# Kernel optimization log

Hardware: AMD Instinct MI355X
Metric: run time of the kernel (lower is better)

## Reference

```python
import jax, jax.numpy as jnp
import numpy as np

DIM, HEADS, HD = 1536, 12, 128
B, F, H, W = 1, 8, 16, 28
L = F * H * W  # 3584
EPS = 1e-6


def setup_inputs() -> dict:
    key = jax.random.key(0)
    ks = jax.random.split(key, 8)
    s = 0.02
    x = jax.random.normal(ks[0], (B, L, DIM), jnp.float32)
    # RoPE tables: angles pos * theta_j, shape [1024, HD//2]
    ang = jnp.arange(1024, dtype=jnp.float32)[:, None] / (
        10000.0 ** (jnp.arange(HD // 2, dtype=jnp.float32) / (HD // 2)))
    freqs_cos = jnp.cos(ang)
    freqs_sin = jnp.sin(ang)
    Wq = jax.random.normal(ks[1], (DIM, DIM), jnp.float32) * s
    Wk = jax.random.normal(ks[2], (DIM, DIM), jnp.float32) * s
    Wv = jax.random.normal(ks[3], (DIM, DIM), jnp.float32) * s
    Wo = jax.random.normal(ks[4], (DIM, DIM), jnp.float32) * s
    zb = jnp.zeros((DIM,), jnp.float32)
    return dict(x=x, freqs_cos=freqs_cos, freqs_sin=freqs_sin,
                Wq=Wq, bq=zb, Wk=Wk, bk=zb, Wv=Wv, bv=zb, Wo=Wo, bo=zb,
                gq=jnp.ones((DIM,), jnp.float32), gk=jnp.ones((DIM,), jnp.float32),
                f=F, h=H, w=W)


def rms_norm(t, g, eps=EPS):
    # WanRMSNorm: x * rsqrt(mean(x^2) + eps) * weight, over last dim (full `dim`)
    return t * jax.lax.rsqrt(jnp.mean(t * t, axis=-1, keepdims=True) + eps) * g


def rope_apply(t, f, h, w, cos, sin):
    # t: [B, L, H, D]; 3D rope with per-axis frequency splits [c-2(c//3), c//3, c//3]
    B_, L_, H_, D_ = t.shape
    c = D_ // 2
    s0 = c - 2 * (c // 3)
    s1 = c // 3

    def build(tab):
        tf = jnp.broadcast_to(tab[:f, :s0][:, None, None, :], (f, h, w, s0))
        th = jnp.broadcast_to(tab[:h, s0:s0 + s1][None, :, None, :], (f, h, w, s1))
        tw = jnp.broadcast_to(tab[:w, s0 + s1:c][None, None, :, :], (f, h, w, s1))
        return jnp.concatenate([tf, th, tw], axis=-1).reshape(f * h * w, c)[:L_]

    cs = build(cos)[None, :, None, :]  # [1, L, 1, c]
    sn = build(sin)[None, :, None, :]
    tp = t.reshape(B_, L_, H_, c, 2)   # consecutive pairs -> complex (re, im)
    tr, ti = tp[..., 0], tp[..., 1]
    out_r = tr * cs - ti * sn
    out_i = tr * sn + ti * cs
    return jnp.stack([out_r, out_i], axis=-1).reshape(B_, L_, H_, D_)


def reference(x, freqs_cos, freqs_sin, Wq, bq, Wk, bk, Wv, bv, Wo, bo, gq, gk, f, h, w):
    B_, L_, _ = x.shape
    q = rms_norm(x @ Wq.T + bq, gq).reshape(B_, L_, HEADS, HD)
    k = rms_norm(x @ Wk.T + bk, gk).reshape(B_, L_, HEADS, HD)
    v = (x @ Wv.T + bv).reshape(B_, L_, HEADS, HD)
    q = rope_apply(q, f, h, w, freqs_cos, freqs_sin)
    k = rope_apply(k, f, h, w, freqs_cos, freqs_sin)
    scale = 1.0 / np.sqrt(HD).astype(np.float32)
    att = jax.nn.softmax(jnp.einsum('bqhd,bkhd->bhqk', q, k) * scale, axis=-1)
    o = jnp.einsum('bhqk,bkhd->bqhd', att, v).reshape(B_, L_, DIM)
    return o @ Wo.T + bo
```

## Files before the change

### kernel.cpp

```cpp
#include <hip/hip_runtime.h>
#include <hip/hip_bf16.h>


#define DIM   1536
#define HEADS 12
#define HD    128
#define LSEQ  3584

typedef __bf16 bf16_t;
typedef __attribute__((ext_vector_type(8))) __bf16 bf16x8;
typedef __attribute__((ext_vector_type(4))) float f32x4;
typedef __attribute__((ext_vector_type(16))) float f32x16;
typedef unsigned int u32;
typedef __attribute__((ext_vector_type(2))) unsigned int u32x2;
typedef __attribute__((ext_vector_type(4))) unsigned int u32x4;

static __device__ __forceinline__ ushort f2bf(float f) {
  bf16_t h = (bf16_t)f;
  return __builtin_bit_cast(ushort, h);
}
static __device__ __forceinline__ float bf2f(ushort u) {
  return (float)__builtin_bit_cast(bf16_t, u);
}
static __device__ __forceinline__ u32 pkbf(float a, float b) {
  return (u32)f2bf(a) | ((u32)f2bf(b) << 16);
}

static __device__ __forceinline__ void plswap(u32& x, u32& y, int hi) {
#if __has_builtin(__builtin_amdgcn_permlane32_swap)
  (void)hi;
  u32x2 r = __builtin_amdgcn_permlane32_swap(x, y, false, false);
  x = r[0]; y = r[1];
#else
  u32 sx = __shfl_xor(x, 32, 64);
  u32 sy = __shfl_xor(y, 32, 64);
  u32 nx = hi ? sy : x;
  u32 ny = hi ? y : sx;
  x = nx; y = ny;
#endif
}

__global__ __launch_bounds__(256) void cvt_f32_bf16(const float* __restrict__ in,
                                                    ushort* __restrict__ out, int n) {
  int i = (blockIdx.x * 256 + threadIdx.x) * 4;
  if (i + 3 < n) {
    float4 v = *reinterpret_cast<const float4*>(in + i);
    ushort4 o;
    o.x = f2bf(v.x); o.y = f2bf(v.y); o.z = f2bf(v.z); o.w = f2bf(v.w);
    *reinterpret_cast<ushort4*>(out + i) = o;
  }
}

template <int SEGS, bool OUT_F32>
__global__ __launch_bounds__(256) void gemm_bt(const ushort* __restrict__ A,
                                               const ushort* __restrict__ B,
                                               const float* __restrict__ bias0,
                                               const float* __restrict__ bias1,
                                               const float* __restrict__ bias2,
                                               void* __restrict__ Cout) {
  const int K = DIM;
  __shared__ __attribute__((aligned(16))) ushort As[128 * 32];
  __shared__ __attribute__((aligned(16))) ushort Bs[128 * 32];
  const int tid  = threadIdx.x;
  const int lane = tid & 63;
  const int wid  = tid >> 6;
  const int m0 = blockIdx.x * 128;
  const int n0 = blockIdx.y * 128;
  const int wm = (wid >> 1) * 64;
  const int wn = (wid & 1) * 64;
  const int lr = lane & 15;
  const int lg = lane >> 4;
  const int crow = lane >> 2;
  const int ccol = (lane & 3) * 8;

  f32x4 acc[4][4] = {};

  for (int kt = 0; kt < K; kt += 32) {
    __syncthreads();
#pragma unroll
    for (int i = 0; i < 2; ++i) {
      int chunk = wid * 2 + i;
      int row = chunk * 16 + crow;
      const ushort* ga = A + (size_t)(m0 + row) * K + kt + ccol;
      const ushort* gb = B + (size_t)(n0 + row) * K + kt + ccol;
      __builtin_amdgcn_global_load_lds(
          (__attribute__((address_space(1))) void*)(void*)ga,
          (__attribute__((address_space(3))) void*)(&As[chunk * 512]), 16, 0, 0);
      __builtin_amdgcn_global_load_lds(
          (__attribute__((address_space(1))) void*)(void*)gb,
          (__attribute__((address_space(3))) void*)(&Bs[chunk * 512]), 16, 0, 0);
    }
    __syncthreads();

    bf16x8 af[4], bfr[4];
#pragma unroll
    for (int m = 0; m < 4; ++m)
      af[m] = *reinterpret_cast<const bf16x8*>(&As[(wm + m * 16 + lr) * 32 + lg * 8]);
#pragma unroll
    for (int n = 0; n < 4; ++n)
      bfr[n] = *reinterpret_cast<const bf16x8*>(&Bs[(wn + n * 16 + lr) * 32 + lg * 8]);
#pragma unroll
    for (int m = 0; m < 4; ++m)
#pragma unroll
      for (int n = 0; n < 4; ++n)
        acc[m][n] = __builtin_amdgcn_mfma_f32_16x16x32_bf16(af[m], bfr[n], acc[m][n], 0, 0, 0);
  }

  int seg = 0;
  const float* bp = bias0;
  if (SEGS == 3) {
    seg = n0 >= 2 * DIM ? 2 : (n0 >= DIM ? 1 : 0);
    bp = seg == 0 ? bias0 : (seg == 1 ? bias1 : bias2);
  }
  const int nbase = n0 - seg * DIM;

#pragma unroll
  for (int m = 0; m < 4; ++m) {
#pragma unroll
    for (int n = 0; n < 4; ++n) {
      int col = nbase + wn + n * 16 + lr;
      float bvv = bp[col];
#pragma unroll
      for (int r = 0; r < 4; ++r) {
        int row = m0 + wm + m * 16 + lg * 4 + r;
        float v = acc[m][n][r] + bvv;
        if (OUT_F32)
          ((float*)Cout)[(size_t)row * DIM + col] = v;
        else
          ((ushort*)Cout)[(size_t)seg * ((size_t)LSEQ * DIM) + (size_t)row * DIM + col] = f2bf(v);
      }
    }
  }
}

__global__ __launch_bounds__(256) void normrope(ushort* __restrict__ Qb,
                                                ushort* __restrict__ Kb,
                                                const float* __restrict__ gq,
                                                const float* __restrict__ gk,
                                                const float* __restrict__ cosT,
                                                const float* __restrict__ sinT) {
  __shared__ float red[4];
  const int l = blockIdx.x;
  const int tid = threadIdx.x;
  ushort* row = (blockIdx.y == 0 ? Qb : Kb) + (size_t)l * DIM;
  const float* g = blockIdx.y == 0 ? gq : gk;

  const u32* rp = reinterpret_cast<const u32*>(row);
  u32 pk[3];
  float v[6];
#pragma unroll
  for (int i = 0; i < 3; ++i) {
    pk[i] = rp[tid * 3 + i];
    v[2 * i]     = bf2f((ushort)(pk[i] & 0xffff));
    v[2 * i + 1] = bf2f((ushort)(pk[i] >> 16));
  }
  float ss = 0.f;
#pragma unroll
  for (int i = 0; i < 6; ++i) ss += v[i] * v[i];
#pragma unroll
  for (int off = 1; off < 64; off <<= 1) ss += __shfl_xor(ss, off, 64);
  if ((tid & 63) == 0) red[tid >> 6] = ss;
  __syncthreads();
  float tot = red[0] + red[1] + red[2] + red[3];
  float rms = rsqrtf(tot * (1.0f / DIM) + 1e-6f);

  const int fi = l / 448;
  const int rem = l % 448;
  const int hi = rem / 28;
  const int wi = rem % 28;

  u32* wp = reinterpret_cast<u32*>(row);
#pragma unroll
  for (int i = 0; i < 3; ++i) {
    int p = tid * 3 + i;
    int head = p >> 6;
    int j = p & 63;
    int trow = (j < 22) ? fi : ((j < 43) ? hi : wi);
    float cv = cosT[trow * 64 + j];
    float sv = sinT[trow * 64 + j];
    int idx = head * 128 + 2 * j;
    float xr = v[2 * i] * rms * g[idx];
    float xi = v[2 * i + 1] * rms * g[idx + 1];
    float orr = xr * cv - xi * sv;
    float oii = xr * sv + xi * cv;
    wp[p] = (u32)f2bf(orr) | ((u32)f2bf(oii) << 16);
  }
}

#define QBLK 128
#define KVB  64

__global__ __launch_bounds__(256, 2) void attn(const ushort* __restrict__ Q,
                                               const ushort* __restrict__ Kp,
                                               const ushort* __restrict__ Vp,
                                               ushort* __restrict__ O,
                                               float* __restrict__ Opart,
                                               float* __restrict__ mlbuf) {
  __shared__ __attribute__((aligned(16))) ushort Ks[2][KVB * 128];
  __shared__ __attribute__((aligned(16))) ushort Vt[2][128][72];
  const int tid  = threadIdx.x;
  const int lane = tid & 63;
  const int wv   = tid >> 6;
  const int lq   = lane & 31;
  const int hi   = lane >> 5;
  const int h    = blockIdx.y;
  const int q0   = blockIdx.x * QBLK;
  const float scale = 0.08838834764831845f;

  const int split  = blockIdx.z;
  const int nsplit = gridDim.z;
  const int NT     = LSEQ / KVB;
  const int t_lo   = split * NT / nsplit;
  const int t_hi   = (split + 1) * NT / nsplit;

  bf16x8 qf[8];
  {
    const ushort* qbase = Q + (size_t)(q0 + wv * 32 + lq) * DIM + h * HD;
#pragma unroll
    for (int d = 0; d < 8; ++d)
      qf[d] = *reinterpret_cast<const bf16x8*>(qbase + d * 16 + hi * 8);
  }

  f32x16 accO[4] = {};
  float m = -1e30f, lsum = 0.f;

  const int mbk = tid >> 4;
  const int mbd = tid & 15;

  uint4 vr0, vr1, vr2, vr3;
  auto issueK = [&](int t, int nb) {
    const int kv0 = t * KVB;
#pragma unroll
    for (int i = 0; i < 4; ++i) {
      int o16 = (wv * 4 + i) * 64 + lane;
      int r = o16 >> 4;
      int b = (o16 & 15) * 16;
      int srcu = (b ^ ((r & 7) << 4)) >> 1;
      const ushort* gp = Kp + (size_t)(kv0 + r) * DIM + h * HD + srcu;
      __builtin_amdgcn_global_load_lds(
          (__attribute__((address_space(1))) void*)(void*)gp,
          (__attribute__((address_space(3))) void*)(&Ks[nb][(wv * 4 + i) * 512]), 16, 0, 0);
    }
  };
  auto loadV = [&](int t) {
    const ushort* vbase = Vp + (size_t)(t * KVB + mbk * 4) * DIM + h * HD + mbd * 8;
    vr0 = *reinterpret_cast<const uint4*>(vbase);
    vr1 = *reinterpret_cast<const uint4*>(vbase + DIM);
    vr2 = *reinterpret_cast<const uint4*>(vbase + 2 * DIM);
    vr3 = *reinterpret_cast<const uint4*>(vbase + 3 * DIM);
  };
  auto writeV = [&](int nb) {
    const ushort* s0 = reinterpret_cast<const ushort*>(&vr0);
    const ushort* s1 = reinterpret_cast<const ushort*>(&vr1);
    const ushort* s2 = reinterpret_cast<const ushort*>(&vr2);
    const ushort* s3 = reinterpret_cast<const ushort*>(&vr3);
#pragma unroll
    for (int jj = 0; jj < 8; ++jj) {
      int j = (jj + mbd) & 7;
      uint2 w;
      w.x = (u32)s0[j] | ((u32)s1[j] << 16);
      w.y = (u32)s2[j] | ((u32)s3[j] << 16);
      *reinterpret_cast<uint2*>(&Vt[nb][mbd * 8 + j][mbk * 4]) = w;
    }
  };

  issueK(t_lo, 0);
  loadV(t_lo);

  int buf = 0;
  for (int t = t_lo; t < t_hi; ++t) {
    writeV(buf);
    __syncthreads();

    if (t + 1 < t_hi) {
      issueK(t + 1, buf ^ 1);
      loadV(t + 1);
    }

#pragma unroll
    for (int hf = 0; hf < 2; ++hf) {
      f32x16 sv = {};
      __builtin_amdgcn_s_setprio(1);
#pragma unroll
      for (int d = 0; d < 8; ++d) {
        int db = d * 32 + hi * 16;
        const bf16x8 a = *reinterpret_cast<const bf16x8*>(
            (const char*)&Ks[buf][0] + (hf * 32 + lq) * 256 + (db ^ ((lq & 7) << 4)));
        sv = __builtin_amdgcn_mfma_f32_32x32x16_bf16(a, qf[d], sv, 0, 0, 0);
      }
      __builtin_amdgcn_s_setprio(0);

      float pmax = sv[0];
#pragma unroll
      for (int r = 1; r < 16; ++r) pmax = fmaxf(pmax, sv[r]);
      pmax = fmaxf(pmax, __shfl_xor(pmax, 32, 64));
      pmax *= scale;

      if (__any(pmax > m + 8.f)) {
        float mn = fmaxf(m, pmax);
        float al = __expf(m - mn);
        m = mn;
        lsum *= al;
#pragma unroll
        for (int r = 0; r < 16; ++r) {
          int qr = (r & 3) + 8 * (r >> 2) + 4 * hi;
          float alr = __shfl(al, qr, 64);
          accO[0][r] *= alr; accO[1][r] *= alr;
          accO[2][r] *= alr; accO[3][r] *= alr;
        }
      }

      float p[16];
      float psum = 0.f;
#pragma unroll
      for (int r = 0; r < 16; ++r) {
        p[r] = __expf(fmaf(sv[r], scale, -m));
        psum += p[r];
      }
      psum += __shfl_xor(psum, 32, 64);
      lsum += psum;

      u32 a0 = pkbf(p[0], p[1]),   a1 = pkbf(p[2], p[3]);
      u32 a4 = pkbf(p[4], p[5]),   a5 = pkbf(p[6], p[7]);
      u32 c0 = pkbf(p[8], p[9]),   c1 = pkbf(p[10], p[11]);
      u32 c4 = pkbf(p[12], p[13]), c5 = pkbf(p[14], p[15]);
      plswap(a0, a4, hi);
      plswap(a1, a5, hi);
      plswap(c0, c4, hi);
      plswap(c1, c5, hi);
      u32x4 w0 = {a0, a1, a4, a5};
      u32x4 w1 = {c0, c1, c4, c5};
      bf16x8 pa0 = __builtin_bit_cast(bf16x8, w0);
      bf16x8 pa1 = __builtin_bit_cast(bf16x8, w1);

      __builtin_amdgcn_s_setprio(1);
#pragma unroll
      for (int nd = 0; nd < 4; ++nd) {
        bf16x8 vb0 = *reinterpret_cast<const bf16x8*>(
            &Vt[buf][nd * 32 + lq][hf * 32 + hi * 8]);
        accO[nd] = __builtin_amdgcn_mfma_f32_32x32x16_bf16(pa0, vb0, accO[nd], 0, 0, 0);
      }
#pragma unroll
      for (int nd = 0; nd < 4; ++nd) {
        bf16x8 vb1 = *reinterpret_cast<const bf16x8*>(
            &Vt[buf][nd * 32 + lq][hf * 32 + 16 + hi * 8]);
        accO[nd] = __builtin_amdgcn_mfma_f32_32x32x16_bf16(pa1, vb1, accO[nd], 0, 0, 0);
      }
      __builtin_amdgcn_s_setprio(0);
    }

    __syncthreads();
    buf ^= 1;
  }

  if (gridDim.z == 1) {
    float inv_own = 1.0f / lsum;
#pragma unroll
    for (int r = 0; r < 16; ++r) {
      int qr = (r & 3) + 8 * (r >> 2) + 4 * hi;
      float inv = __shfl(inv_own, qr, 64);
      ushort* orow = O + (size_t)(q0 + wv * 32 + qr) * DIM + h * HD;
#pragma unroll
      for (int nd = 0; nd < 4; ++nd)
        orow[nd * 32 + lq] = f2bf(accO[nd][r] * inv);
    }
  } else {
    float* Op = Opart + ((size_t)split * HEADS + h) * ((size_t)LSEQ * HD);
#pragma unroll
    for (int r = 0; r < 16; ++r) {
      int qr = (r & 3) + 8 * (r >> 2) + 4 * hi;
      float* orow = Op + (size_t)(q0 + wv * 32 + qr) * HD;
#pragma unroll
      for (int nd = 0; nd < 4; ++nd)
        orow[nd * 32 + lq] = accO[nd][r];
    }
    if (hi == 0) {
      size_t row = (size_t)split * (HEADS * LSEQ) + (size_t)h * LSEQ + (q0 + wv * 32 + lq);
      mlbuf[2 * row]     = m;
      mlbuf[2 * row + 1] = lsum;
    }
  }
}

__global__ __launch_bounds__(256) void attn_merge(const float* __restrict__ Opart,
                                                  const float* __restrict__ mlbuf,
                                                  ushort* __restrict__ Ob, int nsplit) {
  const int RN = HEADS * LSEQ;
  int gi = blockIdx.x * 256 + threadIdx.x;
  int row = gi >> 5;
  int d4 = (gi & 31) * 4;
  if (row >= RN) return;
  int h = row / LSEQ, q = row % LSEQ;

  float M = -1e30f;
  for (int s = 0; s < nsplit; ++s) M = fmaxf(M, mlbuf[2 * ((size_t)s * RN + row)]);
  float den = 0.f;
  float4 acc = {0.f, 0.f, 0.f, 0.f};
  for (int s = 0; s < nsplit; ++s) {
    float ms = mlbuf[2 * ((size_t)s * RN + row)];
    float ls = mlbuf[2 * ((size_t)s * RN + row) + 1];
    float w = __expf(ms - M);
    den += ls * w;
    const float4 o = *reinterpret_cast<const float4*>(
        &Opart[((size_t)s * RN + row) * HD + d4]);
    acc.x += w * o.x; acc.y += w * o.y; acc.z += w * o.z; acc.w += w * o.w;
  }
  float inv = 1.0f / den;
  ushort4 r;
  r.x = f2bf(acc.x * inv); r.y = f2bf(acc.y * inv);
  r.z = f2bf(acc.z * inv); r.w = f2bf(acc.w * inv);
  *reinterpret_cast<ushort4*>(&Ob[(size_t)q * DIM + h * HD + d4]) = r;
}

extern "C" void kernel_launch(void* const* d_in, const int* in_sizes, int n_in,
                              void* d_out, int out_size, void* d_ws, size_t ws_size,
                              hipStream_t stream) {
  (void)in_sizes; (void)n_in; (void)out_size;
  const float* x    = (const float*)d_in[0];
  const float* cosT = (const float*)d_in[1];
  const float* sinT = (const float*)d_in[2];
  const float* Wq   = (const float*)d_in[3];
  const float* bq   = (const float*)d_in[4];
  const float* Wk   = (const float*)d_in[5];
  const float* bk   = (const float*)d_in[6];
  const float* Wv   = (const float*)d_in[7];
  const float* bv_in = (const float*)d_in[8];
  const float* Wo   = (const float*)d_in[9];
  const float* bo   = (const float*)d_in[10];
  const float* gq   = (const float*)d_in[11];
  const float* gk   = (const float*)d_in[12];

  const size_t LD = (size_t)LSEQ * DIM;
  const size_t WD = (size_t)DIM * DIM;
  const size_t base_bytes = (5 * LD + 4 * WD) * sizeof(ushort);
  if (ws_size < base_bytes) return;

  ushort* xb  = (ushort*)d_ws;
  ushort* Wqb = xb + LD;
  ushort* Wkb = Wqb + WD;
  ushort* Wvb = Wkb + WD;
  ushort* Wob = Wvb + WD;
  ushort* Qb  = Wob + WD;
  ushort* Kb  = Qb + LD;
  ushort* Vb  = Kb + LD;
  ushort* Ob  = Vb + LD;

  const size_t RN = (size_t)HEADS * LSEQ;
  const size_t split_bytes = RN * HD * 4 + RN * 8;
  int nsplit = 1;
  if (ws_size >= base_bytes + 3 * split_bytes) nsplit = 3;
  else if (ws_size >= base_bytes + 2 * split_bytes) nsplit = 2;
  float* Opart = (float*)((char*)d_ws + base_bytes);
  float* mlbuf = Opart + (size_t)nsplit * RN * HD;

  cvt_f32_bf16<<<(int)(LD / 4 / 256), 256, 0, stream>>>(x, xb, (int)LD);
  cvt_f32_bf16<<<(int)(WD / 4 / 256), 256, 0, stream>>>(Wq, Wqb, (int)WD);
  cvt_f32_bf16<<<(int)(WD / 4 / 256), 256, 0, stream>>>(Wk, Wkb, (int)WD);
  cvt_f32_bf16<<<(int)(WD / 4 / 256), 256, 0, stream>>>(Wv, Wvb, (int)WD);
  cvt_f32_bf16<<<(int)(WD / 4 / 256), 256, 0, stream>>>(Wo, Wob, (int)WD);

  gemm_bt<3, false><<<dim3(LSEQ / 128, 3 * DIM / 128), 256, 0, stream>>>(
      xb, Wqb, bq, bk, bv_in, Qb);

  normrope<<<dim3(LSEQ, 2), 256, 0, stream>>>(Qb, Kb, gq, gk, cosT, sinT);

  attn<<<dim3(LSEQ / QBLK, HEADS, nsplit), 256, 0, stream>>>(Qb, Kb, Vb, Ob, Opart, mlbuf);
  if (nsplit > 1)
    attn_merge<<<(int)(RN * 32 / 256), 256, 0, stream>>>(Opart, mlbuf, Ob, nsplit);

  gemm_bt<1, true><<<dim3(LSEQ / 128, DIM / 128), 256, 0, stream>>>(
      Ob, Wob, bo, bo, bo, d_out);
}
```

Before: 303.1 us.

## Fuse weight conversions, make GEMM persistent, interleave QK MFMA chains in attention

Merges the four weight fp32->bf16 conversion launches into a single kernel writing contiguous buffers. Turns the projection GEMMs into grid-stride persistent kernels capped at 768 blocks. In attention, computes both 32-key halves of the score tile together, giving two independent MFMA accumulation chains, and uses a tree reduction for the row max. The cost is higher register pressure in attention and a possible tail imbalance in the persistent GEMM.

```diff
diff --git a/kernel.cpp b/kernel.cpp
--- a/kernel.cpp
+++ b/kernel.cpp
@@ -51,6 +51,23 @@
   }
 }
 
+__global__ __launch_bounds__(256) void cvt_w4(const float* __restrict__ s0,
+                                              const float* __restrict__ s1,
+                                              const float* __restrict__ s2,
+                                              const float* __restrict__ s3,
+                                              ushort* __restrict__ dst) {
+  const int WD4 = (DIM * DIM) / 4;
+  const int per = WD4 / 256;
+  int mat = blockIdx.x / per;
+  int rb  = blockIdx.x % per;
+  const float* s = mat == 0 ? s0 : (mat == 1 ? s1 : (mat == 2 ? s2 : s3));
+  int i = (rb * 256 + threadIdx.x) * 4;
+  float4 v = *reinterpret_cast<const float4*>(s + i);
+  ushort4 o;
+  o.x = f2bf(v.x); o.y = f2bf(v.y); o.z = f2bf(v.z); o.w = f2bf(v.w);
+  *reinterpret_cast<ushort4*>(dst + (size_t)mat * DIM * DIM + i) = o;
+}
+
 template <int SEGS, bool OUT_F32>
 __global__ __launch_bounds__(256) void gemm_bt(const ushort* __restrict__ A,
                                                const ushort* __restrict__ B,
@@ -59,13 +76,13 @@
                                                const float* __restrict__ bias2,
                                                void* __restrict__ Cout) {
   const int K = DIM;
+  const int MT = LSEQ / 128;
+  const int ntiles = MT * (SEGS * DIM / 128);
   __shared__ __attribute__((aligned(16))) ushort As[128 * 32];
   __shared__ __attribute__((aligned(16))) ushort Bs[128 * 32];
   const int tid  = threadIdx.x;
   const int lane = tid & 63;
   const int wid  = tid >> 6;
-  const int m0 = blockIdx.x * 128;
-  const int n0 = blockIdx.y * 128;
   const int wm = (wid >> 1) * 64;
   const int wn = (wid & 1) * 64;
   const int lr = lane & 15;
@@ -73,63 +90,69 @@
   const int crow = lane >> 2;
   const int ccol = (lane & 3) * 8;
 
-  f32x4 acc[4][4] = {};
-
-  for (int kt = 0; kt < K; kt += 32) {
+  for (int tile = blockIdx.x; tile < ntiles; tile += gridDim.x) {
+    const int m0 = (tile % MT) * 128;
+    const int n0 = (tile / MT) * 128;
+
+    f32x4 acc[4][4] = {};
+
+    for (int kt = 0; kt < K; kt += 32) {
+      __syncthreads();
+#pragma unroll
+      for (int i = 0; i < 2; ++i) {
+        int chunk = wid * 2 + i;
+        int row = chunk * 16 + crow;
+        const ushort* ga = A + (size_t)(m0 + row) * K + kt + ccol;
+        const ushort* gb = B + (size_t)(n0 + row) * K + kt + ccol;
+        __builtin_amdgcn_global_load_lds(
+            (__attribute__((address_space(1))) void*)(void*)ga,
+            (__attribute__((address_space(3))) void*)(&As[chunk * 512]), 16, 0, 0);
+        __builtin_amdgcn_global_load_lds(
+            (__attribute__((address_space(1))) void*)(void*)gb,
+            (__attribute__((address_space(3))) void*)(&Bs[chunk * 512]), 16, 0, 0);
+      }
+      __syncthreads();
+
+      bf16x8 af[4], bfr[4];
+#pragma unroll
+      for (int m = 0; m < 4; ++m)
+        af[m] = *reinterpret_cast<const bf16x8*>(&As[(wm + m * 16 + lr) * 32 + lg * 8]);
+#pragma unroll
+      for (int n = 0; n < 4; ++n)
+        bfr[n] = *reinterpret_cast<const bf16x8*>(&Bs[(wn + n * 16 + lr) * 32 + lg * 8]);
+#pragma unroll
+      for (int m = 0; m < 4; ++m)
+#pragma unroll
+        for (int n = 0; n < 4; ++n)
+          acc[m][n] = __builtin_amdgcn_mfma_f32_16x16x32_bf16(af[m], bfr[n], acc[m][n], 0, 0, 0);
+    }
+
+    int seg = 0;
+    const float* bp = bias0;
+    if (SEGS == 3) {
+      seg = n0 >= 2 * DIM ? 2 : (n0 >= DIM ? 1 : 0);
+      bp = seg == 0 ? bias0 : (seg == 1 ? bias1 : bias2);
+    }
+    const int nbase = n0 - seg * DIM;
+
+#pragma unroll
+    for (int m = 0; m < 4; ++m) {
+#pragma unroll
+      for (int n = 0; n < 4; ++n) {
+        int col = nbase + wn + n * 16 + lr;
+        float bvv = bp[col];
+#pragma unroll
+        for (int r = 0; r < 4; ++r) {
+          int row = m0 + wm + m * 16 + lg * 4 + r;
+          float v = acc[m][n][r] + bvv;
+          if (OUT_F32)
+            ((float*)Cout)[(size_t)row * DIM + col] = v;
+          else
+            ((ushort*)Cout)[(size_t)seg * ((size_t)LSEQ * DIM) + (size_t)row * DIM + col] = f2bf(v);
+        }
+      }
+    }
     __syncthreads();
-#pragma unroll
-    for (int i = 0; i < 2; ++i) {
-      int chunk = wid * 2 + i;
-      int row = chunk * 16 + crow;
-      const ushort* ga = A + (size_t)(m0 + row) * K + kt + ccol;
-      const ushort* gb = B + (size_t)(n0 + row) * K + kt + ccol;
-      __builtin_amdgcn_global_load_lds(
-          (__attribute__((address_space(1))) void*)(void*)ga,
-          (__attribute__((address_space(3))) void*)(&As[chunk * 512]), 16, 0, 0);
-      __builtin_amdgcn_global_load_lds(
-          (__attribute__((address_space(1))) void*)(void*)gb,
-          (__attribute__((address_space(3))) void*)(&Bs[chunk * 512]), 16, 0, 0);
-    }
-    __syncthreads();
-
-    bf16x8 af[4], bfr[4];
-#pragma unroll
-    for (int m = 0; m < 4; ++m)
-      af[m] = *reinterpret_cast<const bf16x8*>(&As[(wm + m * 16 + lr) * 32 + lg * 8]);
-#pragma unroll
-    for (int n = 0; n < 4; ++n)
-      bfr[n] = *reinterpret_cast<const bf16x8*>(&Bs[(wn + n * 16 + lr) * 32 + lg * 8]);
-#pragma unroll
-    for (int m = 0; m < 4; ++m)
-#pragma unroll
-      for (int n = 0; n < 4; ++n)
-        acc[m][n] = __builtin_amdgcn_mfma_f32_16x16x32_bf16(af[m], bfr[n], acc[m][n], 0, 0, 0);
-  }
-
-  int seg = 0;
-  const float* bp = bias0;
-  if (SEGS == 3) {
-    seg = n0 >= 2 * DIM ? 2 : (n0 >= DIM ? 1 : 0);
-    bp = seg == 0 ? bias0 : (seg == 1 ? bias1 : bias2);
-  }
-  const int nbase = n0 - seg * DIM;
-
-#pragma unroll
-  for (int m = 0; m < 4; ++m) {
-#pragma unroll
-    for (int n = 0; n < 4; ++n) {
-      int col = nbase + wn + n * 16 + lr;
-      float bvv = bp[col];
-#pragma unroll
-      for (int r = 0; r < 4; ++r) {
-        int row = m0 + wm + m * 16 + lg * 4 + r;
-        float v = acc[m][n][r] + bvv;
-        if (OUT_F32)
-          ((float*)Cout)[(size_t)row * DIM + col] = v;
-        else
-          ((ushort*)Cout)[(size_t)seg * ((size_t)LSEQ * DIM) + (size_t)row * DIM + col] = f2bf(v);
-      }
-    }
   }
 }
 
@@ -277,22 +300,31 @@
       loadV(t + 1);
     }
 
+    f32x16 sv0 = {}, sv1 = {};
+    __builtin_amdgcn_s_setprio(1);
+#pragma unroll
+    for (int d = 0; d < 8; ++d) {
+      int db = d * 32 + hi * 16;
+      const bf16x8 a0 = *reinterpret_cast<const bf16x8*>(
+          (const char*)&Ks[buf][0] + lq * 256 + (db ^ ((lq & 7) << 4)));
+      const bf16x8 a1 = *reinterpret_cast<const bf16x8*>(
+          (const char*)&Ks[buf][0] + (32 + lq) * 256 + (db ^ ((lq & 7) << 4)));
+      sv0 = __builtin_amdgcn_mfma_f32_32x32x16_bf16(a0, qf[d], sv0, 0, 0, 0);
+      sv1 = __builtin_amdgcn_mfma_f32_32x32x16_bf16(a1, qf[d], sv1, 0, 0, 0);
+    }
+    __builtin_amdgcn_s_setprio(0);
+
 #pragma unroll
     for (int hf = 0; hf < 2; ++hf) {
-      f32x16 sv = {};
-      __builtin_amdgcn_s_setprio(1);
-#pragma unroll
-      for (int d = 0; d < 8; ++d) {
-        int db = d * 32 + hi * 16;
-        const bf16x8 a = *reinterpret_cast<const bf16x8*>(
-            (const char*)&Ks[buf][0] + (hf * 32 + lq) * 256 + (db ^ ((lq & 7) << 4)));
-        sv = __builtin_amdgcn_mfma_f32_32x32x16_bf16(a, qf[d], sv, 0, 0, 0);
-      }
-      __builtin_amdgcn_s_setprio(0);
-
-      float pmax = sv[0];
-#pragma unroll
-      for (int r = 1; r < 16; ++r) pmax = fmaxf(pmax, sv[r]);
+      const f32x16& sv = hf == 0 ? sv0 : sv1;
+
+      float t01 = fmaxf(sv[0], sv[1]),   t23 = fmaxf(sv[2], sv[3]);
+      float t45 = fmaxf(sv[4], sv[5]),   t67 = fmaxf(sv[6], sv[7]);
+      float t89 = fmaxf(sv[8], sv[9]),   tab = fmaxf(sv[10], sv[11]);
+      float tcd = fmaxf(sv[12], sv[13]), tef = fmaxf(sv[14], sv[15]);
+      float q0m = fmaxf(fmaxf(t01, t23), fmaxf(t45, t67));
+      float q1m = fmaxf(fmaxf(t89, tab), fmaxf(tcd, tef));
+      float pmax = fmaxf(q0m, q1m);
       pmax = fmaxf(pmax, __shfl_xor(pmax, 32, 64));
       pmax *= scale;
 
@@ -437,9 +469,7 @@
 
   ushort* xb  = (ushort*)d_ws;
   ushort* Wqb = xb + LD;
-  ushort* Wkb = Wqb + WD;
-  ushort* Wvb = Wkb + WD;
-  ushort* Wob = Wvb + WD;
+  ushort* Wob = Wqb + 3 * WD;
   ushort* Qb  = Wob + WD;
   ushort* Kb  = Qb + LD;
   ushort* Vb  = Kb + LD;
@@ -454,13 +484,13 @@
   float* mlbuf = Opart + (size_t)nsplit * RN * HD;
 
   cvt_f32_bf16<<<(int)(LD / 4 / 256), 256, 0, stream>>>(x, xb, (int)LD);
-  cvt_f32_bf16<<<(int)(WD / 4 / 256), 256, 0, stream>>>(Wq, Wqb, (int)WD);
-  cvt_f32_bf16<<<(int)(WD / 4 / 256), 256, 0, stream>>>(Wk, Wkb, (int)WD);
-  cvt_f32_bf16<<<(int)(WD / 4 / 256), 256, 0, stream>>>(Wv, Wvb, (int)WD);
-  cvt_f32_bf16<<<(int)(WD / 4 / 256), 256, 0, stream>>>(Wo, Wob, (int)WD);
-
-  gemm_bt<3, false><<<dim3(LSEQ / 128, 3 * DIM / 128), 256, 0, stream>>>(
-      xb, Wqb, bq, bk, bv_in, Qb);
+  cvt_w4<<<(int)(4 * WD / 4 / 256), 256, 0, stream>>>(Wq, Wk, Wv, Wo, Wqb);
+
+  {
+    int nt = (LSEQ / 128) * (3 * DIM / 128);
+    gemm_bt<3, false><<<nt < 768 ? nt : 768, 256, 0, stream>>>(
+        xb, Wqb, bq, bk, bv_in, Qb);
+  }
 
   normrope<<<dim3(LSEQ, 2), 256, 0, stream>>>(Qb, Kb, gq, gk, cosT, sinT);
 
@@ -468,6 +498,9 @@
   if (nsplit > 1)
     attn_merge<<<(int)(RN * 32 / 256), 256, 0, stream>>>(Opart, mlbuf, Ob, nsplit);
 
-  gemm_bt<1, true><<<dim3(LSEQ / 128, DIM / 128), 256, 0, stream>>>(
-      Ob, Wob, bo, bo, bo, d_out);
-}
+  {
+    int nt = (LSEQ / 128) * (DIM / 128);
+    gemm_bt<1, true><<<nt < 768 ? nt : 768, 256, 0, stream>>>(
+        Ob, Wob, bo, bo, bo, d_out);
+  }
+}
```

New measurement: 304.4 us. About the same (+0.4%).
